# Kernel optimization log

Hardware: AMD Instinct MI355X
Metric: run time of the kernel (lower is better)

The kernel has to match this reference:

```python
import jax, jax.numpy as jnp
import numpy as np

L, D, H, DH, W, G, FF = 2, 768, 12, 64, 256, 64, 3072  # W = one-sided window (attention_window=512)
B, S = 2, 4096
NEG = -1e9


def setup_inputs() -> dict:
    key = jax.random.key(0)
    ks = jax.random.split(key, 16)
    inp = {}
    inp['hidden_states'] = jax.random.normal(ks[0], (B, S, D), jnp.float32)
    # HF Longformer convention: <0 masked, >0 global, 0 local. First G tokens are global.
    inp['attention_mask'] = jnp.zeros((B, S), jnp.float32).at[:, :G].set(1.0)
    inp['padding_len'] = 0
    inp['level_hierarchy'] = 0
    def w(k, shape):
        return (jax.random.normal(k, shape, jnp.float32) * 0.02)
    for i, n in enumerate(['Wq', 'Wk', 'Wv', 'Wqg', 'Wkg', 'Wvg', 'Wo']):
        inp[n] = w(ks[1 + i], (L, D, D))
        inp['b' + n[1:].lower()] = jnp.zeros((L, D), jnp.float32)
    inp['Wi'] = w(ks[8], (L, D, FF)); inp['bi'] = jnp.zeros((L, FF), jnp.float32)
    inp['Wo2'] = w(ks[9], (L, FF, D)); inp['bo2'] = jnp.zeros((L, D), jnp.float32)
    for n in ['ln1', 'ln2']:
        inp[n + '_g'] = jnp.ones((L, D), jnp.float32)
        inp[n + '_b'] = jnp.zeros((L, D), jnp.float32)
    return inp


def _ln(x, g, b):
    mu = jnp.mean(x, -1, keepdims=True)
    var = jnp.mean(jnp.square(x - mu), -1, keepdims=True)
    return (x - mu) * jax.lax.rsqrt(var + 1e-5) * g + b


def _chunk3(x, nc, w):
    # x: [..., S, d] -> [..., nc, 3w, d]: keys of chunks (c-1, c, c+1), zero-padded at the ends
    shp = x.shape
    xr = x.reshape(shp[:-2] + (nc, w, shp[-1]))
    pad = [(0, 0)] * xr.ndim
    pad[-3] = (1, 1)
    xp = jnp.pad(xr, pad)
    return jnp.concatenate([xp[..., :-2, :, :], xp[..., 1:-1, :, :], xp[..., 2:, :, :]], axis=-2)


def _layer(h, mask, Wq, bq, Wk, bk, Wv, bv, Wqg, bqg, Wkg, bkg, Wvg, bvg,
           Wo, bo, ln1_g, ln1_b, Wi, bi, Wo2, bo2, ln2_g, ln2_b):
    Bb, Ss, Dd = h.shape
    nc = Ss // W
    scale = 1.0 / np.sqrt(DH)
    def heads(x):
        return x.reshape(Bb, Ss, H, DH).transpose(0, 2, 1, 3)  # [B,H,S,dh]
    q = heads(h @ Wq + bq) * scale
    k = heads(h @ Wk + bk)
    v = heads(h @ Wv + bv)
    # --- sliding-window (banded) attention, chunked ---
    qc = q.reshape(Bb, H, nc, W, DH)
    k3 = _chunk3(k, nc, W)  # [B,H,nc,3W,dh]
    v3 = _chunk3(v, nc, W)
    local = jnp.einsum('bhcid,bhcjd->bhcij', qc, k3)  # [B,H,nc,W,3W]
    i = jnp.arange(W)[:, None]
    j = jnp.arange(3 * W)[None, :]
    band_ok = jnp.abs(j - W - i) <= W                              # [W,3W]
    keypos = jnp.arange(nc)[:, None, None] * W + (j - W)[None]     # [nc,1,3W]
    in_range = (keypos >= 0) & (keypos < Ss)
    # masked and global keys are removed from the windowed attention (handled via global cols)
    key_local = _chunk3((mask == 0).astype(h.dtype)[..., None], nc, W)[..., 0] > 0.5  # [B,nc,3W]
    valid = band_ok[None, None] & in_range[None] & key_local[:, :, None, :]  # [B,nc,W,3W]
    local = jnp.where(valid[:, None], local, NEG)
    # --- global key columns (every token attends to the G global tokens) ---
    kg, vg = k[:, :, :G], v[:, :, :G]
    sg = jnp.einsum('bhsd,bhgd->bhsg', q, kg).reshape(Bb, H, nc, W, G)
    probs = jax.nn.softmax(jnp.concatenate([sg, local], axis=-1), axis=-1)
    pg, pl = probs[..., :G], probs[..., G:]
    out = (jnp.einsum('bhcig,bhgd->bhcid', pg, vg)
           + jnp.einsum('bhcij,bhcjd->bhcid', pl, v3)).reshape(Bb, H, Ss, DH)
    # --- global token rows: full attention with dedicated global projections ---
    qg = heads(h @ Wqg + bqg)[:, :, :G] * scale
    kgf = heads(h @ Wkg + bkg)
    vgf = heads(h @ Wvg + bvg)
    add = jnp.where(mask < 0, NEG, 0.0)[:, None, None, :]
    pgl = jax.nn.softmax(jnp.einsum('bhgd,bhsd->bhgs', qg, kgf) + add, axis=-1)
    out = out.at[:, :, :G].set(jnp.einsum('bhgs,bhsd->bhgd', pgl, vgf))
    out = jnp.where((mask < 0)[:, None, :, None], 0.0, out)
    attn = out.transpose(0, 2, 1, 3).reshape(Bb, Ss, Dd) @ Wo + bo
    h = _ln(attn + h, ln1_g, ln1_b)
    ff = jax.nn.gelu(h @ Wi + bi, approximate=False) @ Wo2 + bo2
    return _ln(ff + h, ln2_g, ln2_b)


def reference(hidden_states, attention_mask, padding_len, level_hierarchy,
              Wq, bq, Wk, bk, Wv, bv, Wqg, bqg, Wkg, bkg, Wvg, bvg,
              Wo, bo, ln1_g, ln1_b, Wi, bi, Wo2, bo2, ln2_g, ln2_b):
    h = hidden_states
    for l in range(L):
        h = _layer(h, attention_mask,
                   Wq[l], bq[l], Wk[l], bk[l], Wv[l], bv[l],
                   Wqg[l], bqg[l], Wkg[l], bkg[l], Wvg[l], bvg[l],
                   Wo[l], bo[l], ln1_g[l], ln1_b[l],
                   Wi[l], bi[l], Wo2[l], bo2[l], ln2_g[l], ln2_b[l])
    if padding_len > 0:
        h = h[:, :-padding_len]
    return h
```

## Files before the change

### kernel.cpp

```cpp
#include <hip/hip_runtime.h>

#define B_ 2
#define S_ 4096
#define D_ 768
#define H_ 12
#define DH_ 64
#define W_ 256
#define G_ 64
#define FF_ 3072
#define L_ 2
#define M_ (B_*S_)
#define NEGV -1e9f
#define NSPLIT 16

typedef short bf16x8 __attribute__((ext_vector_type(8)));
typedef float f32x4 __attribute__((ext_vector_type(4)));
typedef unsigned short u16;
typedef unsigned short u16x4 __attribute__((ext_vector_type(4)));

__device__ __forceinline__ u16 f2bf(float f) {
  union { float f; unsigned u; } a; a.f = f;
  unsigned r = a.u + 0x7FFFu + ((a.u >> 16) & 1u);
  return (u16)(r >> 16);
}
__device__ __forceinline__ float b2f(u16 u) {
  union { unsigned u; float f; } a; a.u = ((unsigned)u) << 16;
  return a.f;
}

__device__ __forceinline__ f32x4 mfma16(bf16x8 a, bf16x8 b, f32x4 c) {
  return __builtin_amdgcn_mfma_f32_16x16x32_bf16(a, b, c, 0, 0, 0);
}

__device__ __forceinline__ void gload16(const u16* g, u16* l) {
  __builtin_amdgcn_global_load_lds((const __attribute__((address_space(1))) void*)g,
                                   (__attribute__((address_space(3))) void*)l, 16, 0, 0);
}

__device__ __forceinline__ int xcd_swz(int bid, int nwg) {
  if ((nwg & 7) == 0) {
    int cpx = nwg >> 3;
    bid = (bid & 7) * cpx + (bid >> 3);
  }
  return bid;
}

struct Ptr7 { const float* p[7]; };
__global__ __launch_bounds__(256) void wtrans7(Ptr7 in, u16* __restrict__ out) {
  __shared__ float tile[32][33];
  int z = blockIdx.z;
  int slab = z >> 1, l = z & 1;
  const float* src = in.p[slab] + (size_t)l * D_ * D_;
  u16* dst = out + (size_t)z * D_ * D_;
  int k0 = blockIdx.y * 32, n0 = blockIdx.x * 32;
  int tx = threadIdx.x, ty = threadIdx.y;
#pragma unroll
  for (int i = 0; i < 4; i++)
    tile[ty + i*8][tx] = src[(size_t)(k0 + ty + i*8) * D_ + n0 + tx];
  __syncthreads();
#pragma unroll
  for (int i = 0; i < 4; i++)
    dst[(size_t)(n0 + ty + i*8) * D_ + k0 + tx] = f2bf(tile[tx][ty + i*8]);
}

__global__ __launch_bounds__(256) void wtrans(const float* __restrict__ in,
                                              u16* __restrict__ out, int K, int N) {
  __shared__ float tile[32][33];
  size_t base = (size_t)blockIdx.z * K * N;
  int k0 = blockIdx.y * 32, n0 = blockIdx.x * 32;
  int tx = threadIdx.x, ty = threadIdx.y;
#pragma unroll
  for (int i = 0; i < 4; i++)
    tile[ty + i*8][tx] = in[base + (size_t)(k0 + ty + i*8) * N + n0 + tx];
  __syncthreads();
#pragma unroll
  for (int i = 0; i < 4; i++)
    out[base + (size_t)(n0 + ty + i*8) * K + k0 + tx] = f2bf(tile[tx][ty + i*8]);
}

__global__ __launch_bounds__(256) void conv_b(const float* __restrict__ in,
                                              u16* __restrict__ outb, int n4) {
  int i = blockIdx.x * 256 + threadIdx.x;
  if (i >= n4) return;
  float4 v = ((const float4*)in)[i];
  u16x4 o;
  o[0] = f2bf(v.x); o[1] = f2bf(v.y); o[2] = f2bf(v.z); o[3] = f2bf(v.w);
  ((u16x4*)outb)[i] = o;
}

template <int MODE>
__device__ __forceinline__ float epi_post(float v) {
  if (MODE == 2) return v * 0.125f;
  if (MODE == 3) {
    float y = 0.79788456f * (v + 0.044715f * v * v * v);
    float e = __expf(fminf(2.f * y, 20.f));
    return v * e / (e + 1.f);
  }
  return v;
}

struct Bias5 { const float* p[5]; };

#define VMC4() asm volatile("s_waitcnt vmcnt(4)" ::: "memory")
#define VMC0() asm volatile("s_waitcnt vmcnt(0)" ::: "memory")
#define GPH_PRE() do { __builtin_amdgcn_s_barrier(); \
  asm volatile("s_waitcnt lgkmcnt(0)" ::: "memory"); \
  __builtin_amdgcn_sched_barrier(0); } while (0)
#define GPH_PRE_NOLDS() do { __builtin_amdgcn_s_barrier(); \
  __builtin_amdgcn_sched_barrier(0); } while (0)
#define GPH_POST() do { __builtin_amdgcn_sched_barrier(0); \
  __builtin_amdgcn_s_barrier(); } while (0)
#define GPH_MFMA(AF, BF, QM, QN) do { \
  __builtin_amdgcn_s_setprio(1); \
  _Pragma("unroll") for (int mi = 0; mi < 4; mi++) \
  _Pragma("unroll") for (int nj = 0; nj < 2; nj++) \
  _Pragma("unroll") for (int ks = 0; ks < 2; ks++) \
    acc[(QM)*4+mi][(QN)*2+nj] = mfma16(AF[mi][ks], BF[nj][ks], acc[(QM)*4+mi][(QN)*2+nj]); \
  __builtin_amdgcn_s_setprio(0); } while (0)

template <int MODE, int NW>
__global__ __launch_bounds__(512, 2) void gemm256p(const u16* __restrict__ A,
                                                   const u16* __restrict__ Wbase,
                                                   Bias5 bp,
                                                   u16* __restrict__ OutBase,
                                                   int Kdim, int Nstride, int l) {
  __shared__ u16 sh[65536];
  int gx = gridDim.x;
  int bid = blockIdx.x + blockIdx.y * gx;
  bid = xcd_swz(bid, gx * gridDim.y);
  int bxx = bid % gx, by = bid / gx;
  int bm = by * 256;
  int widx, bn;
  const u16* Bt; u16* Cb; const float* bias;
  if (NW == 5) {
    widx = bxx / 3;
    bn = (bxx % 3) * 256;
    int slab = widx + (widx >= 3 ? 1 : 0);
    Bt = Wbase + ((size_t)slab * L_ + l) * (size_t)D_ * D_;
    Cb = OutBase + (size_t)slab * M_ * D_;
    bias = bp.p[widx];
  } else {
    widx = 0;
    bn = bxx * 256;
    Bt = Wbase; Cb = OutBase; bias = bp.p[0];
  }
  int tid = threadIdx.x;
  int lane = tid & 63, wid = tid >> 6;
  int wr = wid >> 2, wc = wid & 3;
  int lr = lane & 15, lg = lane >> 4;

  int rr0 = tid >> 3, slot0 = tid & 7;
  int c80 = slot0 ^ (rr0 & 7);
  const u16* pA = A + (size_t)(bm + rr0) * Kdim + c80 * 8;
  const u16* pB = Bt + (size_t)(bn + rr0) * Kdim + c80 * 8;

  auto stA = [&](int buf, int h, int kt) {
    u16* base = sh + buf * 16384;
    gload16(pA + (size_t)(h * 128) * Kdim + kt * 64, &base[(h * 1024 + tid) * 8]);
    gload16(pA + (size_t)(h * 128 + 64) * Kdim + kt * 64, &base[(h * 1024 + 512 + tid) * 8]);
  };
  auto stB = [&](int buf, int h, int kt) {
    u16* base = sh + 32768 + buf * 16384;
    gload16(pB + (size_t)(h * 128) * Kdim + kt * 64, &base[(h * 1024 + tid) * 8]);
    gload16(pB + (size_t)(h * 128 + 64) * Kdim + kt * 64, &base[(h * 1024 + 512 + tid) * 8]);
  };
  auto ldA = [&](bf16x8 (&af)[4][2], int c, int qm) {
    const u16* base = sh + c * 16384;
#pragma unroll
    for (int mi = 0; mi < 4; mi++)
#pragma unroll
      for (int ks = 0; ks < 2; ks++) {
        int row = wr * 128 + qm * 64 + mi * 16 + lr;
        int c8 = ks * 4 + lg;
        af[mi][ks] = *(const bf16x8*)&base[(row * 8 + (c8 ^ (row & 7))) * 8];
      }
  };
  auto ldB = [&](bf16x8 (&bf)[2][2], int c, int qn) {
    const u16* base = sh + 32768 + c * 16384;
#pragma unroll
    for (int nj = 0; nj < 2; nj++)
#pragma unroll
      for (int ks = 0; ks < 2; ks++) {
        int row = wc * 64 + qn * 32 + nj * 16 + lr;
        int c8 = ks * 4 + lg;
        bf[nj][ks] = *(const bf16x8*)&base[(row * 8 + (c8 ^ (row & 7))) * 8];
      }
  };

  f32x4 acc[8][4] = {};
  int nt = Kdim >> 6;

  stA(0, 0, 0); stA(0, 1, 0);
  stB(0, 0, 0); stB(0, 1, 0);
  stB(1, 0, 1); stB(1, 1, 1);
  VMC4();
  __builtin_amdgcn_s_barrier();

  bf16x8 af[4][2], b0[2][2], b1[2][2];
  for (int kt = 0; kt < nt; kt += 2) {
    bool notlast = (kt + 2 < nt);
    ldA(af, 0, 0); ldB(b0, 0, 0);
    stA(1, 0, kt + 1);
    GPH_PRE(); GPH_MFMA(af, b0, 0, 0); GPH_POST();
    ldB(b1, 0, 1);
    stA(1, 1, kt + 1);
    GPH_PRE(); GPH_MFMA(af, b1, 0, 1); GPH_POST();
    ldA(af, 0, 1);
    if (notlast) stB(0, 0, kt + 2);
    GPH_PRE(); GPH_MFMA(af, b0, 1, 0); GPH_POST();
    if (notlast) { stB(0, 1, kt + 2); VMC4(); } else { VMC0(); }
    GPH_PRE_NOLDS(); GPH_MFMA(af, b1, 1, 1); GPH_POST();
    ldA(af, 1, 0); ldB(b0, 1, 0);
    if (notlast) stA(0, 0, kt + 2);
    GPH_PRE(); GPH_MFMA(af, b0, 0, 0); GPH_POST();
    ldB(b1, 1, 1);
    if (notlast) stA(0, 1, kt + 2);
    GPH_PRE(); GPH_MFMA(af, b1, 0, 1); GPH_POST();
    ldA(af, 1, 1);
    if (notlast) stB(1, 0, kt + 3);
    GPH_PRE(); GPH_MFMA(af, b0, 1, 0); GPH_POST();
    if (notlast) { stB(1, 1, kt + 3); VMC4(); } else { VMC0(); }
    GPH_PRE_NOLDS(); GPH_MFMA(af, b1, 1, 1); GPH_POST();
  }

  int r0 = bm + wr * 128, c0 = bn + wc * 64;
  int cr = (lane >> 4) * 4, cc = lane & 15;
  float sc = (NW == 5 && widx == 0) ? 0.125f : 1.0f;
#pragma unroll
  for (int nj = 0; nj < 4; nj++) {
    int col = c0 + nj * 16 + cc;
    float bv = bias[col];
#pragma unroll
    for (int mi = 0; mi < 8; mi++)
#pragma unroll
      for (int r = 0; r < 4; r++) {
        size_t off = (size_t)(r0 + mi * 16 + cr + r) * Nstride + col;
        Cb[off] = f2bf(epi_post<MODE>((acc[mi][nj][r] + bv) * sc));
      }
  }
}

template <int MODE>
__global__ __launch_bounds__(256) void gemm_pipe(const u16* __restrict__ A,
                                                 const u16* __restrict__ Bt,
                                                 const float* __restrict__ bias,
                                                 u16* __restrict__ Cb,
                                                 int Ndim, int Kdim, int rowTileStride) {
  __shared__ u16 sh[24576];
  int gx = gridDim.x;
  int bid = blockIdx.x + blockIdx.y * gx;
  bid = xcd_swz(bid, gx * gridDim.y);
  int bm = (bid / gx) * rowTileStride * 128;
  int bn = (bid % gx) * 128;
  int tid = threadIdx.x;
  int lane = tid & 63, w = tid >> 6;
  int r0w = (w >> 1) * 64, c0w = (w & 1) * 64;
  int lr = lane & 15, lg = lane >> 4;

  int f0 = tid, l0 = f0 >> 3, s0 = (f0 & 7) ^ (l0 & 7);
  int row0 = (l0 << 1) | (s0 >> 2), c0s = (s0 & 3) * 8;
  int f1 = tid + 256, l1 = f1 >> 3, s1 = (f1 & 7) ^ (l1 & 7);
  int row1 = (l1 << 1) | (s1 >> 2), c1s = (s1 & 3) * 8;
  const u16* A0 = A + (size_t)(bm + row0) * Kdim + c0s;
  const u16* A1 = A + (size_t)(bm + row1) * Kdim + c1s;
  const u16* B0 = Bt + (size_t)(bn + row0) * Kdim + c0s;
  const u16* B1 = Bt + (size_t)(bn + row1) * Kdim + c1s;

  int offa[4], offb[4];
#pragma unroll
  for (int i = 0; i < 4; i++) {
    int ra = r0w + i * 16 + lr;
    int la = ra >> 1, sa = ((ra & 1) << 2) | lg;
    offa[i] = la * 64 + (sa ^ (la & 7)) * 8;
    int rb = c0w + i * 16 + lr;
    int lb = rb >> 1, sb = ((rb & 1) << 2) | lg;
    offb[i] = lb * 64 + (sb ^ (lb & 7)) * 8;
  }

  auto stage = [&](int kt, int buf) {
    int k1 = kt << 5;
    u16* ab = sh + buf * 4096;
    u16* bb = sh + 12288 + buf * 4096;
    gload16(A0 + k1, &ab[tid * 8]);
    gload16(A1 + k1, &ab[tid * 8 + 2048]);
    gload16(B0 + k1, &bb[tid * 8]);
    gload16(B1 + k1, &bb[tid * 8 + 2048]);
  };

  int nt = Kdim >> 5;
  f32x4 acc[4][4] = {};

  stage(0, 0);
  if (nt > 1) stage(1, 1);

  for (int t = 0; t < nt; t++) {
    int cb = t % 3;
    if (t + 2 < nt) {
      stage(t + 2, (t + 2) % 3);
      asm volatile("s_waitcnt vmcnt(8)" ::: "memory");
    } else if (t + 1 < nt) {
      asm volatile("s_waitcnt vmcnt(4)" ::: "memory");
    } else {
      asm volatile("s_waitcnt vmcnt(0)" ::: "memory");
    }
    __builtin_amdgcn_s_barrier();
    __builtin_amdgcn_sched_barrier(0);
    const u16* ab = sh + cb * 4096;
    const u16* bb = sh + 12288 + cb * 4096;
    bf16x8 a[4], b[4];
#pragma unroll
    for (int i = 0; i < 4; i++) a[i] = *(const bf16x8*)&ab[offa[i]];
#pragma unroll
    for (int j = 0; j < 4; j++) b[j] = *(const bf16x8*)&bb[offb[j]];
#pragma unroll
    for (int i = 0; i < 4; i++)
#pragma unroll
      for (int j = 0; j < 4; j++)
        acc[i][j] = mfma16(a[i], b[j], acc[i][j]);
    __builtin_amdgcn_sched_barrier(0);
    __builtin_amdgcn_s_barrier();
    __builtin_amdgcn_sched_barrier(0);
  }

  int cr = (lane >> 4) * 4, cc = lane & 15;
#pragma unroll
  for (int j = 0; j < 4; j++) {
    int col = c0w + j * 16 + cc;
    float bv = bias[bn + col];
#pragma unroll
    for (int i = 0; i < 4; i++)
#pragma unroll
      for (int r = 0; r < 4; r++) {
        int row = r0w + i * 16 + cr + r;
        int chunk = (col >> 3) ^ (row & 15);
        sh[row * 128 + chunk * 8 + (col & 7)] =
            f2bf(epi_post<MODE>(acc[i][j][r] + bv));
      }
  }
  __syncthreads();
  {
    int row = tid >> 1, half = tid & 1;
    u16* gro = Cb + (size_t)(bm + row) * Ndim + bn + half * 64;
#pragma unroll
    for (int c = 0; c < 8; c++) {
      int lc = half * 8 + c;
      int pc = lc ^ (row & 15);
      bf16x8 v = *(const bf16x8*)&sh[row * 128 + pc * 8];
      *(bf16x8*)(gro + c * 8) = v;
    }
  }
}

__global__ __launch_bounds__(128) void attn_local(const u16* __restrict__ qb,
                                                  const u16* __restrict__ kb_,
                                                  const u16* __restrict__ vb,
                                                  const float* __restrict__ mask,
                                                  u16* __restrict__ ao) {
  int bid = blockIdx.x + blockIdx.y * gridDim.x;
  bid = xcd_swz(bid, 1536);
  int cx = bid & 63, bh = bid >> 6;
  int c = cx >> 2, sub = cx & 3;
  int b = bh / H_, h = bh % H_;
  int tid = threadIdx.x;
  int w = tid >> 6, lane = tid & 63;
  int lr = lane & 15, lg = lane >> 4;

  __shared__ u16 vtT[64][72];
  __shared__ u16 plds[2][32][72];
  __shared__ unsigned char vflag[576];

  int base_off = sub * 64;
  int kwin0 = c * W_ - W_;
  for (int i = tid; i < 576; i += 128) {
    int kp = kwin0 + base_off + i;
    vflag[i] = (kp >= 0 && kp < S_ && mask[b * S_ + kp] == 0.0f) ? 1 : 0;
  }

  size_t hoff = (size_t)b * S_ * D_ + h * DH_;
  int qrow0 = c * W_ + base_off + w * 32;
  bf16x8 aq[2][2];
#pragma unroll
  for (int fi = 0; fi < 2; fi++)
#pragma unroll
    for (int ks = 0; ks < 2; ks++)
      aq[fi][ks] = *(const bf16x8*)(qb + hoff + (size_t)(qrow0 + fi * 16 + lr) * D_ + ks * 32 + lg * 8);

  int K0 = kwin0 + base_off;
  int kb_lo = (K0 < 0) ? (1 + ((-K0) >> 6)) : 1;
  int kb_hi = 9;
  { int hi = 1 + ((S_ - 64 - K0) >> 6); if (hi < 9) kb_hi = hi; }
  int niter = 1 + (kb_hi - kb_lo + 1);

  int stg_k4 = tid >> 3, stg_j = tid & 7;
  int stg_dh0 = stg_j * 8;

  float ls[2][4];
  f32x4 o[2][4] = {};
#pragma unroll
  for (int fi = 0; fi < 2; fi++)
#pragma unroll
    for (int r = 0; r < 4; r++) ls[fi][r] = 0.f;

  bf16x8 ck0[4], ck1[4], nk0[4], nk1[4], cv[4], nv[4];
#pragma unroll
  for (int nj = 0; nj < 4; nj++) {
    const u16* ks8 = kb_ + hoff + (size_t)(nj * 16 + lr) * D_ + lg * 8;
    ck0[nj] = *(const bf16x8*)(ks8);
    ck1[nj] = *(const bf16x8*)(ks8 + 32);
  }
#pragma unroll
  for (int p = 0; p < 4; p++)
    cv[p] = *(const bf16x8*)(vb + hoff + (size_t)(p * 16 + stg_k4) * D_ + stg_dh0);

  for (int it = 0; it < niter; it++) {
    int kb = (it == 0) ? 0 : (kb_lo + it - 1);

    __builtin_amdgcn_s_barrier();
#pragma unroll
    for (int p = 0; p < 4; p++) {
      int key = p * 16 + stg_k4;
      u16* basep = &vtT[stg_dh0][key ^ (stg_j << 3)];
#pragma unroll
      for (int e = 0; e < 8; e++) basep[e * 72] = (u16)cv[p][e];
    }
    if (it + 1 < niter) {
      int kb2 = kb_lo + it;
      int ks2 = K0 + (kb2 - 1) * 64;
#pragma unroll
      for (int nj = 0; nj < 4; nj++) {
        const u16* ks8 = kb_ + hoff + (size_t)(ks2 + nj * 16 + lr) * D_ + lg * 8;
        nk0[nj] = *(const bf16x8*)(ks8);
        nk1[nj] = *(const bf16x8*)(ks8 + 32);
      }
#pragma unroll
      for (int p = 0; p < 4; p++)
        nv[p] = *(const bf16x8*)(vb + hoff + (size_t)(ks2 + p * 16 + stg_k4) * D_ + stg_dh0);
    }
    asm volatile("s_waitcnt lgkmcnt(0)" ::: "memory");
    __builtin_amdgcn_s_barrier();
    __builtin_amdgcn_sched_barrier(0);

    f32x4 sc[2][4];
#pragma unroll
    for (int fi = 0; fi < 2; fi++)
#pragma unroll
      for (int nj = 0; nj < 4; nj++) {
        f32x4 t = {};
        t = mfma16(aq[fi][0], ck0[nj], t);
        t = mfma16(aq[fi][1], ck1[nj], t);
        sc[fi][nj] = t;
      }

    if (kb >= 2 && kb <= 8) {
#pragma unroll
      for (int nj = 0; nj < 4; nj++) {
        bool kv = vflag[(kb - 1) * 64 + nj * 16 + lr] != 0;
#pragma unroll
        for (int fi = 0; fi < 2; fi++)
#pragma unroll
          for (int r = 0; r < 4; r++)
            sc[fi][nj][r] = kv ? sc[fi][nj][r] : NEGV;
      }
    } else if (kb > 0) {
#pragma unroll
      for (int nj = 0; nj < 4; nj++) {
        int fidx = (kb - 1) * 64 + nj * 16 + lr;
        int koff = base_off + fidx;
        bool kv = vflag[fidx] != 0;
#pragma unroll
        for (int fi = 0; fi < 2; fi++)
#pragma unroll
          for (int r = 0; r < 4; r++) {
            int wq = base_off + w * 32 + fi * 16 + lg * 4 + r;
            if (!(kv && koff >= wq && koff <= wq + 2 * W_)) sc[fi][nj][r] = NEGV;
          }
      }
    }

#pragma unroll
    for (int fi = 0; fi < 2; fi++)
#pragma unroll
      for (int r = 0; r < 4; r++) {
        float ps = 0.f;
#pragma unroll
        for (int nj = 0; nj < 4; nj++) {
          float p = __expf(sc[fi][nj][r]);
          sc[fi][nj][r] = p;
          ps += p;
        }
#pragma unroll
        for (int d = 1; d < 16; d <<= 1) ps += __shfl_xor(ps, d);
        ls[fi][r] += ps;
      }

#pragma unroll
    for (int fi = 0; fi < 2; fi++)
#pragma unroll
      for (int nj = 0; nj < 4; nj++)
#pragma unroll
        for (int r = 0; r < 4; r++)
          plds[w][fi * 16 + lg * 4 + r][nj * 16 + lr] = f2bf(sc[fi][nj][r]);
    asm volatile("s_waitcnt lgkmcnt(0)" ::: "memory");
    __builtin_amdgcn_sched_barrier(0);

    bf16x8 ap[2][2];
#pragma unroll
    for (int fi = 0; fi < 2; fi++)
#pragma unroll
      for (int ks = 0; ks < 2; ks++)
        ap[fi][ks] = *(const bf16x8*)&plds[w][fi * 16 + lr][ks * 32 + lg * 8];
#pragma unroll
    for (int dj = 0; dj < 4; dj++) {
      int xr = ((dj * 16 + lr) >> 3) & 7;
#pragma unroll
      for (int ks = 0; ks < 2; ks++) {
        bf16x8 bv = *(const bf16x8*)&vtT[dj * 16 + lr][(ks * 32 + lg * 8) ^ (xr << 3)];
        o[0][dj] = mfma16(ap[0][ks], bv, o[0][dj]);
        o[1][dj] = mfma16(ap[1][ks], bv, o[1][dj]);
      }
    }

    if (it + 1 < niter) {
#pragma unroll
      for (int j = 0; j < 4; j++) {
        ck0[j] = nk0[j]; ck1[j] = nk1[j]; cv[j] = nv[j];
      }
    }
  }

#pragma unroll
  for (int fi = 0; fi < 2; fi++)
#pragma unroll
    for (int dj = 0; dj < 4; dj++)
#pragma unroll
      for (int r = 0; r < 4; r++) {
        int row = qrow0 + fi * 16 + lg * 4 + r;
        float v = o[fi][dj][r] / ls[fi][r];
        ao[hoff + (size_t)row * D_ + dj * 16 + lr] = f2bf(v);
      }
}

__global__ __launch_bounds__(128) void attn_gsplit(const u16* __restrict__ qg,
                                                   const u16* __restrict__ kg,
                                                   const u16* __restrict__ vg,
                                                   float* __restrict__ opart,
                                                   float* __restrict__ lpart) {
  int sp = blockIdx.x, bh = blockIdx.y;
  int b = bh / H_, h = bh % H_;
  int tid = threadIdx.x, w = tid >> 6, lane = tid & 63;
  int lr = lane & 15, lg = lane >> 4;
  __shared__ u16 vtT[64][72];
  __shared__ u16 plds[2][32][72];
  size_t hoff = (size_t)b * S_ * D_ + h * DH_;
  int qrow0 = w * 32;
  bf16x8 aq[2][2];
#pragma unroll
  for (int fi = 0; fi < 2; fi++)
#pragma unroll
    for (int ks = 0; ks < 2; ks++)
      aq[fi][ks] = *(const bf16x8*)(qg + hoff + (size_t)(qrow0 + fi * 16 + lr) * D_ + ks * 32 + lg * 8);
  float ls[2][4];
  f32x4 o[2][4] = {};
#pragma unroll
  for (int fi = 0; fi < 2; fi++)
#pragma unroll
    for (int r = 0; r < 4; r++) ls[fi][r] = 0.f;

  int stg_k4 = tid >> 3, stg_j = tid & 7;
  int stg_dh0 = stg_j * 8;

  for (int kb = 0; kb < 4; kb++) {
    int kstart = sp * 256 + kb * 64;
    __syncthreads();
#pragma unroll
    for (int p = 0; p < 4; p++) {
      int key = p * 16 + stg_k4;
      bf16x8 row = *(const bf16x8*)(vg + hoff + (size_t)(kstart + key) * D_ + stg_dh0);
      u16* basep = &vtT[stg_dh0][key ^ (stg_j << 3)];
#pragma unroll
      for (int e = 0; e < 8; e++) basep[e * 72] = (u16)row[e];
    }
    __syncthreads();

    bf16x8 bk0[4], bk1[4];
#pragma unroll
    for (int nj = 0; nj < 4; nj++) {
      const u16* ks8 = kg + hoff + (size_t)(kstart + nj * 16 + lr) * D_ + lg * 8;
      bk0[nj] = *(const bf16x8*)(ks8);
      bk1[nj] = *(const bf16x8*)(ks8 + 32);
    }
    f32x4 sc[2][4];
#pragma unroll
    for (int fi = 0; fi < 2; fi++)
#pragma unroll
      for (int nj = 0; nj < 4; nj++) {
        f32x4 t = {};
        t = mfma16(aq[fi][0], bk0[nj], t);
        t = mfma16(aq[fi][1], bk1[nj], t);
        sc[fi][nj] = t;
      }
#pragma unroll
    for (int fi = 0; fi < 2; fi++)
#pragma unroll
      for (int r = 0; r < 4; r++) {
        float ps = 0.f;
#pragma unroll
        for (int nj = 0; nj < 4; nj++) {
          float p = __expf(sc[fi][nj][r]);
          sc[fi][nj][r] = p;
          ps += p;
        }
#pragma unroll
        for (int d = 1; d < 16; d <<= 1) ps += __shfl_xor(ps, d);
        ls[fi][r] += ps;
      }
#pragma unroll
    for (int fi = 0; fi < 2; fi++)
#pragma unroll
      for (int nj = 0; nj < 4; nj++)
#pragma unroll
        for (int r = 0; r < 4; r++)
          plds[w][fi * 16 + lg * 4 + r][nj * 16 + lr] = f2bf(sc[fi][nj][r]);
    asm volatile("s_waitcnt lgkmcnt(0)" ::: "memory");
    __builtin_amdgcn_sched_barrier(0);
    bf16x8 ap[2][2];
#pragma unroll
    for (int fi = 0; fi < 2; fi++)
#pragma unroll
      for (int ks = 0; ks < 2; ks++)
        ap[fi][ks] = *(const bf16x8*)&plds[w][fi * 16 + lr][ks * 32 + lg * 8];
#pragma unroll
    for (int dj = 0; dj < 4; dj++) {
      int xr = ((dj * 16 + lr) >> 3) & 7;
#pragma unroll
      for (int ks = 0; ks < 2; ks++) {
        bf16x8 bv = *(const bf16x8*)&vtT[dj * 16 + lr][(ks * 32 + lg * 8) ^ (xr << 3)];
        o[0][dj] = mfma16(ap[0][ks], bv, o[0][dj]);
        o[1][dj] = mfma16(ap[1][ks], bv, o[1][dj]);
      }
    }
  }

  size_t pbase = (size_t)(bh * NSPLIT + sp) * 64;
#pragma unroll
  for (int fi = 0; fi < 2; fi++)
#pragma unroll
    for (int r = 0; r < 4; r++) {
      int row = qrow0 + fi * 16 + lg * 4 + r;
      if (lr == 0) lpart[pbase + row] = ls[fi][r];
#pragma unroll
      for (int dj = 0; dj < 4; dj++)
        opart[(pbase + row) * 64 + dj * 16 + lr] = o[fi][dj][r];
    }
}

__global__ __launch_bounds__(256) void attn_gcombine(const float* __restrict__ opart,
                                                     const float* __restrict__ lpart,
                                                     u16* __restrict__ ao) {
  int bh = blockIdx.x;
  int b = bh / H_, h = bh % H_;
  int t = threadIdx.x;
  __shared__ float lt[64];
  if (t < 64) {
    float lsum = 0.f;
#pragma unroll
    for (int sp = 0; sp < NSPLIT; sp++)
      lsum += lpart[(size_t)(bh * NSPLIT + sp) * 64 + t];
    lt[t] = lsum;
  }
  __syncthreads();
  int row = t >> 2, c0 = (t & 3) * 16;
  float acc[16] = {};
  for (int sp = 0; sp < NSPLIT; sp++) {
    const float* op = opart + ((size_t)(bh * NSPLIT + sp) * 64 + row) * 64 + c0;
#pragma unroll
    for (int j = 0; j < 16; j++) acc[j] += op[j];
  }
  float inv = 1.f / lt[row];
  size_t hoff = (size_t)b * S_ * D_ + h * DH_;
#pragma unroll
  for (int j = 0; j < 16; j++)
    ao[hoff + (size_t)row * D_ + c0 + j] = f2bf(acc[j] * inv);
}

__global__ __launch_bounds__(192) void ln_b(const u16* __restrict__ x,
                                            const u16* __restrict__ res,
                                            const float* __restrict__ gg,
                                            const float* __restrict__ bb,
                                            u16* __restrict__ outb,
                                            float* __restrict__ outf) {
  int row = blockIdx.x, t = threadIdx.x;
  const u16* xr = x + (size_t)row * D_;
  const u16* rr = res + (size_t)row * D_;
  u16x4 xv = *(const u16x4*)&xr[t * 4];
  u16x4 rv = *(const u16x4*)&rr[t * 4];
  float v[4];
#pragma unroll
  for (int e = 0; e < 4; e++) v[e] = b2f(xv[e]) + b2f(rv[e]);
  __shared__ float sha[3], shb[3];
  float s = v[0] + v[1] + v[2] + v[3];
#pragma unroll
  for (int d = 1; d < 64; d <<= 1) s += __shfl_xor(s, d);
  if ((t & 63) == 0) sha[t >> 6] = s;
  __syncthreads();
  float mu = (sha[0] + sha[1] + sha[2]) * (1.f / 768.f);
  float dd[4], s2 = 0.f;
#pragma unroll
  for (int e = 0; e < 4; e++) { dd[e] = v[e] - mu; s2 += dd[e] * dd[e]; }
#pragma unroll
  for (int d = 1; d < 64; d <<= 1) s2 += __shfl_xor(s2, d);
  if ((t & 63) == 0) shb[t >> 6] = s2;
  __syncthreads();
  float var = (shb[0] + shb[1] + shb[2]) * (1.f / 768.f);
  float rs = rsqrtf(var + 1e-5f);
  float4 gv = *(const float4*)&gg[t * 4];
  float4 bv = *(const float4*)&bb[t * 4];
  float y0 = dd[0] * rs * gv.x + bv.x;
  float y1 = dd[1] * rs * gv.y + bv.y;
  float y2 = dd[2] * rs * gv.z + bv.z;
  float y3 = dd[3] * rs * gv.w + bv.w;
  u16x4 ov;
  ov[0] = f2bf(y0); ov[1] = f2bf(y1); ov[2] = f2bf(y2); ov[3] = f2bf(y3);
  *(u16x4*)&outb[(size_t)row * D_ + t * 4] = ov;
  if (outf) {
    float4 of = {y0, y1, y2, y3};
    *(float4*)&outf[(size_t)row * D_ + t * 4] = of;
  }
}

extern "C" void kernel_launch(void* const* d_in, const int* in_sizes, int n_in,
                              void* d_out, int out_size, void* d_ws, size_t ws_size,
                              hipStream_t stream) {
  (void)in_sizes; (void)n_in; (void)out_size; (void)ws_size;
  const float* hidden = (const float*)d_in[0];
  const float* mask   = (const float*)d_in[1];
  const float* Wq  = (const float*)d_in[4];   const float* bq  = (const float*)d_in[5];
  const float* Wk  = (const float*)d_in[6];   const float* bk  = (const float*)d_in[7];
  const float* Wv  = (const float*)d_in[8];   const float* bv  = (const float*)d_in[9];
  const float* Wqg = (const float*)d_in[10];  const float* bqg = (const float*)d_in[11];
  const float* Wkg = (const float*)d_in[12];  const float* bkg = (const float*)d_in[13];
  const float* Wvg = (const float*)d_in[14];  const float* bvg = (const float*)d_in[15];
  const float* Wo  = (const float*)d_in[16];  const float* bo  = (const float*)d_in[17];
  const float* Wi  = (const float*)d_in[18];  const float* bi  = (const float*)d_in[19];
  const float* Wo2 = (const float*)d_in[20];  const float* bo2 = (const float*)d_in[21];
  const float* ln1g = (const float*)d_in[22]; const float* ln1b = (const float*)d_in[23];
  const float* ln2g = (const float*)d_in[24]; const float* ln2b = (const float*)d_in[25];

  char* ws = (char*)d_ws;
  size_t off = 0;
  auto alloc = [&](size_t bytes) -> void* {
    void* p = ws + off;
    off += (bytes + 255) & ~(size_t)255;
    return p;
  };
  const size_t DD = (size_t)D_ * D_;
  const size_t DF = (size_t)D_ * FF_;
  u16* Wt = (u16*)alloc((7 * L_ * DD + 2 * L_ * DF) * 2);
  u16* wqg_t = Wt + 3 * L_ * DD;
  u16* wo_t  = Wt + 6 * L_ * DD;
  u16* wi_t  = Wt + 7 * L_ * DD;
  u16* wo2_t = Wt + 7 * L_ * DD + L_ * DF;

  u16* X0 = (u16*)alloc((size_t)M_ * D_ * 2);
  u16* X1 = (u16*)alloc((size_t)M_ * D_ * 2);
  u16* tb = (u16*)alloc((size_t)M_ * D_ * 2);
  u16* B_bf = (u16*)alloc((size_t)M_ * FF_ * 2);
  u16* qbf  = (u16*)alloc((size_t)M_ * D_ * 2);
  u16* kbf  = (u16*)alloc((size_t)M_ * D_ * 2);
  u16* vbf  = (u16*)alloc((size_t)M_ * D_ * 2);
  u16* qgbf = (u16*)alloc((size_t)M_ * D_ * 2);
  u16* kgbf = (u16*)alloc((size_t)M_ * D_ * 2);
  u16* vgbf = (u16*)alloc((size_t)M_ * D_ * 2);
  u16* aobf = (u16*)alloc((size_t)M_ * D_ * 2);
  float* opart = (float*)alloc((size_t)B_ * H_ * NSPLIT * 64 * 64 * 4);
  float* lpart = (float*)alloc((size_t)B_ * H_ * NSPLIT * 64 * 4);

  dim3 tb32(32, 8);
  Ptr7 wp;
  wp.p[0] = Wq; wp.p[1] = Wk; wp.p[2] = Wv; wp.p[3] = Wqg;
  wp.p[4] = Wkg; wp.p[5] = Wvg; wp.p[6] = Wo;
  wtrans7<<<dim3(24, 24, 14), tb32, 0, stream>>>(wp, Wt);
  wtrans<<<dim3(96, 24, 2), tb32, 0, stream>>>(Wi,  wi_t,  D_, FF_);
  wtrans<<<dim3(24, 96, 2), tb32, 0, stream>>>(Wo2, wo2_t, FF_, D_);

  conv_b<<<(M_ * D_ / 4 + 255) / 256, 256, 0, stream>>>(hidden, X0, M_ * D_ / 4);

  for (int l = 0; l < L_; l++) {
    size_t wdd = (size_t)l * DD;
    size_t wdf = (size_t)l * DF;
    dim3 g64(6, 64), g2(6, 2);

    Bias5 bp;
    bp.p[0] = bq  + l * D_;
    bp.p[1] = bk  + l * D_;
    bp.p[2] = bv  + l * D_;
    bp.p[3] = bkg + l * D_;
    bp.p[4] = bvg + l * D_;
    gemm256p<1, 5><<<dim3(15, 32), 512, 0, stream>>>(X0, Wt, bp, qbf, D_, D_, l);
    gemm_pipe<2><<<g2, 256, 0, stream>>>(X0, wqg_t + wdd, bqg + l * D_, qgbf, D_, D_, 32);

    attn_local<<<dim3((S_ / W_) * 4, B_ * H_), 128, 0, stream>>>(qbf, kbf, vbf, mask, aobf);
    attn_gsplit<<<dim3(NSPLIT, B_ * H_), 128, 0, stream>>>(qgbf, kgbf, vgbf, opart, lpart);
    attn_gcombine<<<B_ * H_, 256, 0, stream>>>(opart, lpart, aobf);

    gemm_pipe<1><<<g64, 256, 0, stream>>>(aobf, wo_t + wdd, bo + l * D_, tb, D_, D_, 1);
    ln_b<<<M_, 192, 0, stream>>>(tb, X0, ln1g + l * D_, ln1b + l * D_, X1, nullptr);

    Bias5 bpi; bpi.p[0] = bi + l * FF_;
    gemm256p<3, 1><<<dim3(12, 32), 512, 0, stream>>>(X1, wi_t + wdf, bpi, B_bf, D_, FF_, 0);
    gemm_pipe<1><<<g64, 256, 0, stream>>>(B_bf, wo2_t + wdf, bo2 + l * D_, tb, D_, FF_, 1);

    ln_b<<<M_, 192, 0, stream>>>(tb, X1, ln2g + l * D_, ln2b + l * D_, X0,
                                 (l == L_ - 1) ? (float*)d_out : nullptr);
  }
}
```

Before: 688.7 us.

## Replace 256x256 GEMM with 128x256 triple-buffered tile and fold global-Q GEMM in

Swaps the 256x256 ping-pong GEMM kernel for a 128x256-tile kernel with K-step 32, a three-stage LDS ring buffer, and up to four blocks per CU. The global-query projection is folded into the same launch as a sixth weight slab, computed only for the row tiles that hold the global tokens, which removes a separate low-occupancy gemm_pipe launch. The aim is more resident blocks and better load balance. The cost is less data reuse per tile and more barriers per K step.

```diff
diff --git a/kernel.cpp b/kernel.cpp
--- a/kernel.cpp
+++ b/kernel.cpp
@@ -99,43 +99,34 @@
   return v;
 }
 
-struct Bias5 { const float* p[5]; };
-
-#define VMC4() asm volatile("s_waitcnt vmcnt(4)" ::: "memory")
-#define VMC0() asm volatile("s_waitcnt vmcnt(0)" ::: "memory")
-#define GPH_PRE() do { __builtin_amdgcn_s_barrier(); \
-  asm volatile("s_waitcnt lgkmcnt(0)" ::: "memory"); \
-  __builtin_amdgcn_sched_barrier(0); } while (0)
-#define GPH_PRE_NOLDS() do { __builtin_amdgcn_s_barrier(); \
-  __builtin_amdgcn_sched_barrier(0); } while (0)
-#define GPH_POST() do { __builtin_amdgcn_sched_barrier(0); \
-  __builtin_amdgcn_s_barrier(); } while (0)
-#define GPH_MFMA(AF, BF, QM, QN) do { \
-  __builtin_amdgcn_s_setprio(1); \
-  _Pragma("unroll") for (int mi = 0; mi < 4; mi++) \
-  _Pragma("unroll") for (int nj = 0; nj < 2; nj++) \
-  _Pragma("unroll") for (int ks = 0; ks < 2; ks++) \
-    acc[(QM)*4+mi][(QN)*2+nj] = mfma16(AF[mi][ks], BF[nj][ks], acc[(QM)*4+mi][(QN)*2+nj]); \
-  __builtin_amdgcn_s_setprio(0); } while (0)
+struct Bias6 { const float* p[6]; };
 
 template <int MODE, int NW>
-__global__ __launch_bounds__(512, 2) void gemm256p(const u16* __restrict__ A,
-                                                   const u16* __restrict__ Wbase,
-                                                   Bias5 bp,
-                                                   u16* __restrict__ OutBase,
-                                                   int Kdim, int Nstride, int l) {
-  __shared__ u16 sh[65536];
+__global__ __launch_bounds__(512, 4) void gemm_wide(const u16* __restrict__ A,
+                                                    const u16* __restrict__ Wbase,
+                                                    Bias6 bp,
+                                                    u16* __restrict__ OutBase,
+                                                    int Kdim, int Nstride, int l) {
+  __shared__ u16 sh[36864];
   int gx = gridDim.x;
   int bid = blockIdx.x + blockIdx.y * gx;
   bid = xcd_swz(bid, gx * gridDim.y);
   int bxx = bid % gx, by = bid / gx;
-  int bm = by * 256;
+  int bm = by * 128;
   int widx, bn;
   const u16* Bt; u16* Cb; const float* bias;
+  bool qscale = false;
   if (NW == 5) {
     widx = bxx / 3;
     bn = (bxx % 3) * 256;
-    int slab = widx + (widx >= 3 ? 1 : 0);
+    int slab;
+    if (widx == 5) {
+      if (by != 0 && by != 32) return;
+      slab = 3; qscale = true;
+    } else {
+      slab = widx + (widx >= 3 ? 1 : 0);
+      qscale = (widx == 0);
+    }
     Bt = Wbase + ((size_t)slab * L_ + l) * (size_t)D_ * D_;
     Cb = OutBase + (size_t)slab * M_ * D_;
     bias = bp.p[widx];
@@ -149,93 +140,86 @@
   int wr = wid >> 2, wc = wid & 3;
   int lr = lane & 15, lg = lane >> 4;
 
-  int rr0 = tid >> 3, slot0 = tid & 7;
-  int c80 = slot0 ^ (rr0 & 7);
-  const u16* pA = A + (size_t)(bm + rr0) * Kdim + c80 * 8;
-  const u16* pB = Bt + (size_t)(bn + rr0) * Kdim + c80 * 8;
-
-  auto stA = [&](int buf, int h, int kt) {
-    u16* base = sh + buf * 16384;
-    gload16(pA + (size_t)(h * 128) * Kdim + kt * 64, &base[(h * 1024 + tid) * 8]);
-    gload16(pA + (size_t)(h * 128 + 64) * Kdim + kt * 64, &base[(h * 1024 + 512 + tid) * 8]);
+  int fA = tid;
+  int lA_ = fA >> 3, uA = (fA & 7) ^ (lA_ & 7);
+  int rowA = lA_ * 2 + (uA >> 2), c8A = uA & 3;
+  const u16* srcA = A + (size_t)(bm + rowA) * Kdim + c8A * 8;
+  int fB0 = tid, fB1 = tid + 512;
+  int lB0 = fB0 >> 3, uB0 = (fB0 & 7) ^ (lB0 & 7);
+  int rB0 = lB0 * 2 + (uB0 >> 2), c8B0 = uB0 & 3;
+  int lB1 = fB1 >> 3, uB1 = (fB1 & 7) ^ (lB1 & 7);
+  int rB1 = lB1 * 2 + (uB1 >> 2), c8B1 = uB1 & 3;
+  const u16* srcB0 = Bt + (size_t)(bn + rB0) * Kdim + c8B0 * 8;
+  const u16* srcB1 = Bt + (size_t)(bn + rB1) * Kdim + c8B1 * 8;
+
+  auto stage = [&](int kt, int buf) {
+    int k1 = kt << 5;
+    gload16(srcA + k1, &sh[buf * 4096 + fA * 8]);
+    gload16(srcB0 + k1, &sh[12288 + buf * 8192 + fB0 * 8]);
+    gload16(srcB1 + k1, &sh[12288 + buf * 8192 + fB1 * 8]);
   };
-  auto stB = [&](int buf, int h, int kt) {
-    u16* base = sh + 32768 + buf * 16384;
-    gload16(pB + (size_t)(h * 128) * Kdim + kt * 64, &base[(h * 1024 + tid) * 8]);
-    gload16(pB + (size_t)(h * 128 + 64) * Kdim + kt * 64, &base[(h * 1024 + 512 + tid) * 8]);
-  };
-  auto ldA = [&](bf16x8 (&af)[4][2], int c, int qm) {
-    const u16* base = sh + c * 16384;
-#pragma unroll
-    for (int mi = 0; mi < 4; mi++)
-#pragma unroll
-      for (int ks = 0; ks < 2; ks++) {
-        int row = wr * 128 + qm * 64 + mi * 16 + lr;
-        int c8 = ks * 4 + lg;
-        af[mi][ks] = *(const bf16x8*)&base[(row * 8 + (c8 ^ (row & 7))) * 8];
-      }
-  };
-  auto ldB = [&](bf16x8 (&bf)[2][2], int c, int qn) {
-    const u16* base = sh + 32768 + c * 16384;
-#pragma unroll
-    for (int nj = 0; nj < 2; nj++)
-#pragma unroll
-      for (int ks = 0; ks < 2; ks++) {
-        int row = wc * 64 + qn * 32 + nj * 16 + lr;
-        int c8 = ks * 4 + lg;
-        bf[nj][ks] = *(const bf16x8*)&base[(row * 8 + (c8 ^ (row & 7))) * 8];
-      }
-  };
-
-  f32x4 acc[8][4] = {};
-  int nt = Kdim >> 6;
-
-  stA(0, 0, 0); stA(0, 1, 0);
-  stB(0, 0, 0); stB(0, 1, 0);
-  stB(1, 0, 1); stB(1, 1, 1);
-  VMC4();
-  __builtin_amdgcn_s_barrier();
-
-  bf16x8 af[4][2], b0[2][2], b1[2][2];
-  for (int kt = 0; kt < nt; kt += 2) {
-    bool notlast = (kt + 2 < nt);
-    ldA(af, 0, 0); ldB(b0, 0, 0);
-    stA(1, 0, kt + 1);
-    GPH_PRE(); GPH_MFMA(af, b0, 0, 0); GPH_POST();
-    ldB(b1, 0, 1);
-    stA(1, 1, kt + 1);
-    GPH_PRE(); GPH_MFMA(af, b1, 0, 1); GPH_POST();
-    ldA(af, 0, 1);
-    if (notlast) stB(0, 0, kt + 2);
-    GPH_PRE(); GPH_MFMA(af, b0, 1, 0); GPH_POST();
-    if (notlast) { stB(0, 1, kt + 2); VMC4(); } else { VMC0(); }
-    GPH_PRE_NOLDS(); GPH_MFMA(af, b1, 1, 1); GPH_POST();
-    ldA(af, 1, 0); ldB(b0, 1, 0);
-    if (notlast) stA(0, 0, kt + 2);
-    GPH_PRE(); GPH_MFMA(af, b0, 0, 0); GPH_POST();
-    ldB(b1, 1, 1);
-    if (notlast) stA(0, 1, kt + 2);
-    GPH_PRE(); GPH_MFMA(af, b1, 0, 1); GPH_POST();
-    ldA(af, 1, 1);
-    if (notlast) stB(1, 0, kt + 3);
-    GPH_PRE(); GPH_MFMA(af, b0, 1, 0); GPH_POST();
-    if (notlast) { stB(1, 1, kt + 3); VMC4(); } else { VMC0(); }
-    GPH_PRE_NOLDS(); GPH_MFMA(af, b1, 1, 1); GPH_POST();
-  }
-
-  int r0 = bm + wr * 128, c0 = bn + wc * 64;
+
+  int offa[4], offb[4];
+#pragma unroll
+  for (int i = 0; i < 4; i++) {
+    int ra = wr * 64 + i * 16 + lr;
+    int la = ra >> 1, sa = (((ra & 1) << 2) | lg) ^ (la & 7);
+    offa[i] = la * 64 + sa * 8;
+    int rb = wc * 64 + i * 16 + lr;
+    int lb = rb >> 1, sb = (((rb & 1) << 2) | lg) ^ (lb & 7);
+    offb[i] = lb * 64 + sb * 8;
+  }
+
+  int nt = Kdim >> 5;
+  f32x4 acc[4][4] = {};
+
+  stage(0, 0);
+  if (nt > 1) stage(1, 1);
+
+  for (int t = 0; t < nt; t++) {
+    int cb = t % 3;
+    if (t + 2 < nt) {
+      stage(t + 2, (t + 2) % 3);
+      asm volatile("s_waitcnt vmcnt(6)" ::: "memory");
+    } else if (t + 1 < nt) {
+      asm volatile("s_waitcnt vmcnt(3)" ::: "memory");
+    } else {
+      asm volatile("s_waitcnt vmcnt(0)" ::: "memory");
+    }
+    __builtin_amdgcn_s_barrier();
+    __builtin_amdgcn_sched_barrier(0);
+    const u16* ab = sh + cb * 4096;
+    const u16* bb = sh + 12288 + cb * 8192;
+    bf16x8 a[4], b[4];
+#pragma unroll
+    for (int i = 0; i < 4; i++) a[i] = *(const bf16x8*)&ab[offa[i]];
+#pragma unroll
+    for (int j = 0; j < 4; j++) b[j] = *(const bf16x8*)&bb[offb[j]];
+    __builtin_amdgcn_s_setprio(1);
+#pragma unroll
+    for (int i = 0; i < 4; i++)
+#pragma unroll
+      for (int j = 0; j < 4; j++)
+        acc[i][j] = mfma16(a[i], b[j], acc[i][j]);
+    __builtin_amdgcn_s_setprio(0);
+    __builtin_amdgcn_sched_barrier(0);
+    __builtin_amdgcn_s_barrier();
+    __builtin_amdgcn_sched_barrier(0);
+  }
+
+  int r0 = bm + wr * 64, c0 = bn + wc * 64;
   int cr = (lane >> 4) * 4, cc = lane & 15;
-  float sc = (NW == 5 && widx == 0) ? 0.125f : 1.0f;
-#pragma unroll
-  for (int nj = 0; nj < 4; nj++) {
-    int col = c0 + nj * 16 + cc;
+  float sc = qscale ? 0.125f : 1.0f;
+#pragma unroll
+  for (int j = 0; j < 4; j++) {
+    int col = c0 + j * 16 + cc;
     float bv = bias[col];
 #pragma unroll
-    for (int mi = 0; mi < 8; mi++)
+    for (int i = 0; i < 4; i++)
 #pragma unroll
       for (int r = 0; r < 4; r++) {
-        size_t off = (size_t)(r0 + mi * 16 + cr + r) * Nstride + col;
-        Cb[off] = f2bf(epi_post<MODE>((acc[mi][nj][r] + bv) * sc));
+        size_t off = (size_t)(r0 + i * 16 + cr + r) * Nstride + col;
+        Cb[off] = f2bf(epi_post<MODE>((acc[i][j][r] + bv) * sc));
       }
   }
 }
@@ -756,7 +740,6 @@
   const size_t DD = (size_t)D_ * D_;
   const size_t DF = (size_t)D_ * FF_;
   u16* Wt = (u16*)alloc((7 * L_ * DD + 2 * L_ * DF) * 2);
-  u16* wqg_t = Wt + 3 * L_ * DD;
   u16* wo_t  = Wt + 6 * L_ * DD;
   u16* wi_t  = Wt + 7 * L_ * DD;
   u16* wo2_t = Wt + 7 * L_ * DD + L_ * DF;
@@ -765,12 +748,12 @@
   u16* X1 = (u16*)alloc((size_t)M_ * D_ * 2);
   u16* tb = (u16*)alloc((size_t)M_ * D_ * 2);
   u16* B_bf = (u16*)alloc((size_t)M_ * FF_ * 2);
-  u16* qbf  = (u16*)alloc((size_t)M_ * D_ * 2);
-  u16* kbf  = (u16*)alloc((size_t)M_ * D_ * 2);
-  u16* vbf  = (u16*)alloc((size_t)M_ * D_ * 2);
-  u16* qgbf = (u16*)alloc((size_t)M_ * D_ * 2);
-  u16* kgbf = (u16*)alloc((size_t)M_ * D_ * 2);
-  u16* vgbf = (u16*)alloc((size_t)M_ * D_ * 2);
+  u16* qbf  = (u16*)alloc((size_t)M_ * D_ * 2 * 6);
+  u16* kbf  = qbf + 1 * (size_t)M_ * D_;
+  u16* vbf  = qbf + 2 * (size_t)M_ * D_;
+  u16* qgbf = qbf + 3 * (size_t)M_ * D_;
+  u16* kgbf = qbf + 4 * (size_t)M_ * D_;
+  u16* vgbf = qbf + 5 * (size_t)M_ * D_;
   u16* aobf = (u16*)alloc((size_t)M_ * D_ * 2);
   float* opart = (float*)alloc((size_t)B_ * H_ * NSPLIT * 64 * 64 * 4);
   float* lpart = (float*)alloc((size_t)B_ * H_ * NSPLIT * 64 * 4);
@@ -788,16 +771,16 @@
   for (int l = 0; l < L_; l++) {
     size_t wdd = (size_t)l * DD;
     size_t wdf = (size_t)l * DF;
-    dim3 g64(6, 64), g2(6, 2);
-
-    Bias5 bp;
+    dim3 g64(6, 64);
+
+    Bias6 bp;
     bp.p[0] = bq  + l * D_;
     bp.p[1] = bk  + l * D_;
     bp.p[2] = bv  + l * D_;
     bp.p[3] = bkg + l * D_;
     bp.p[4] = bvg + l * D_;
-    gemm256p<1, 5><<<dim3(15, 32), 512, 0, stream>>>(X0, Wt, bp, qbf, D_, D_, l);
-    gemm_pipe<2><<<g2, 256, 0, stream>>>(X0, wqg_t + wdd, bqg + l * D_, qgbf, D_, D_, 32);
+    bp.p[5] = bqg + l * D_;
+    gemm_wide<1, 5><<<dim3(18, 64), 512, 0, stream>>>(X0, Wt, bp, qbf, D_, D_, l);
 
     attn_local<<<dim3((S_ / W_) * 4, B_ * H_), 128, 0, stream>>>(qbf, kbf, vbf, mask, aobf);
     attn_gsplit<<<dim3(NSPLIT, B_ * H_), 128, 0, stream>>>(qgbf, kgbf, vgbf, opart, lpart);
@@ -806,8 +789,8 @@
     gemm_pipe<1><<<g64, 256, 0, stream>>>(aobf, wo_t + wdd, bo + l * D_, tb, D_, D_, 1);
     ln_b<<<M_, 192, 0, stream>>>(tb, X0, ln1g + l * D_, ln1b + l * D_, X1, nullptr);
 
-    Bias5 bpi; bpi.p[0] = bi + l * FF_;
-    gemm256p<3, 1><<<dim3(12, 32), 512, 0, stream>>>(X1, wi_t + wdf, bpi, B_bf, D_, FF_, 0);
+    Bias6 bpi; bpi.p[0] = bi + l * FF_;
+    gemm_wide<3, 1><<<dim3(12, 64), 512, 0, stream>>>(X1, wi_t + wdf, bpi, B_bf, D_, FF_, 0);
     gemm_pipe<1><<<g64, 256, 0, stream>>>(B_bf, wo2_t + wdf, bo2 + l * D_, tb, D_, FF_, 1);
 
     ln_b<<<M_, 192, 0, stream>>>(tb, X1, ln2g + l * D_, ln2b + l * D_, X0,
```

Measured after the change: 650.1 us. -5.6%, faster.
